# Performance work log

Hardware: AMD Instinct MI355X
Metric: run time of the kernel (lower is better)

The kernel has to match this reference:

```python
import jax, jax.numpy as jnp
import numpy as np

EMBED_DIM = 1024
NUM_HEADS = 16
HEAD_DIM = EMBED_DIM // NUM_HEADS


def setup_inputs() -> dict:
    key = jax.random.key(0)
    ks = jax.random.split(key, 5)
    s = 0.02
    return {
        "x": jax.random.normal(ks[0], (2, 2048, EMBED_DIM), dtype=jnp.float32),
        "w_qkv": jax.random.normal(ks[1], (EMBED_DIM, 3 * EMBED_DIM), dtype=jnp.float32) * s,
        "b_qkv": jnp.zeros((3 * EMBED_DIM,), dtype=jnp.float32),
        "w_out": jax.random.normal(ks[2], (EMBED_DIM, EMBED_DIM), dtype=jnp.float32) * s,
        "b_out": jnp.zeros((EMBED_DIM,), dtype=jnp.float32),
    }


def reference(x, w_qkv, b_qkv, w_out, b_out):
    B, T, C = x.shape
    qkv = x @ w_qkv + b_qkv                       # [B,T,3C]
    q, k, v = jnp.split(qkv, 3, axis=-1)
    # [B,T,C] -> [B,H,T,Dh]
    def heads(t):
        return t.reshape(B, T, NUM_HEADS, HEAD_DIM).transpose(0, 2, 1, 3)
    q, k, v = heads(q), heads(k), heads(v)
    scale = 1.0 / np.sqrt(HEAD_DIM).astype(np.float32)
    scores = jnp.einsum("bhqd,bhkd->bhqk", q, k) * scale  # [B,H,T,T]
    causal = jnp.tril(jnp.ones((T, T), dtype=bool))
    scores = jnp.where(causal[None, None], scores, -jnp.inf)
    attn = jax.nn.softmax(scores, axis=-1)
    out = jnp.einsum("bhqk,bhkd->bhqd", attn, v)  # [B,H,T,Dh]
    out = out.transpose(0, 2, 1, 3).reshape(B, T, C)
    return out @ w_out + b_out
```

## Files before the change

### kernel.cpp

```cpp
#include <hip/hip_runtime.h>

typedef unsigned short u16;
typedef unsigned int u32;
typedef __attribute__((ext_vector_type(8))) short bf16x8;
typedef __attribute__((ext_vector_type(4))) float f32x4;
typedef __attribute__((ext_vector_type(16))) float f32x16;

#define TOK   4096
#define EMB   1024
#define NQKV  3072
#define TSEQ  2048
#define NH    16

__device__ __forceinline__ u16 f2b(float f) {
  union { float f; unsigned u; } v; v.f = f;
  unsigned r = v.u + 0x7FFFu + ((v.u >> 16) & 1u);
  return (u16)(r >> 16);
}

__device__ __forceinline__ u32 pack_rn(float a, float b) {
  u32 ua = __float_as_uint(a) + 0x8000u;
  u32 ub = __float_as_uint(b) + 0x8000u;
  return __builtin_amdgcn_perm(ub, ua, 0x07060302u);
}

__device__ __forceinline__ f32x16 zero16() {
  f32x16 z;
#pragma unroll
  for (int i = 0; i < 16; i++) z[i] = 0.f;
  return z;
}


__global__ __launch_bounds__(256) void prep_kernel(const float* __restrict__ x,
                                                   u16* __restrict__ x_bf,
                                                   const float* __restrict__ w_qkv,
                                                   u16* __restrict__ wqkvT,
                                                   const float* __restrict__ w_out,
                                                   u16* __restrict__ woutT) {
  __shared__ u16 sm[64][65];
  int bid = blockIdx.x, tid = threadIdx.x;
  if (bid < 4096) {
    int i = bid * 256 + tid;
    float4 v = ((const float4*)x)[i];
    union { u16 us[4]; uint2 u2; } o;
    o.us[0] = f2b(v.x); o.us[1] = f2b(v.y); o.us[2] = f2b(v.z); o.us[3] = f2b(v.w);
    ((uint2*)x_bf)[i] = o.u2;
    return;
  }
  const float* src; u16* dst; int R, C, bx, by;
  if (bid < 4096 + 768) {
    int t = bid - 4096; bx = t % 48; by = t / 48;
    src = w_qkv; dst = wqkvT; R = EMB; C = NQKV;
  } else {
    int t = bid - 4096 - 768; bx = t & 15; by = t >> 4;
    src = w_out; dst = woutT; R = EMB; C = EMB;
  }
  int c0 = bx * 64, r0 = by * 64;
#pragma unroll
  for (int i = 0; i < 16; i++) {
    int idx = tid + i * 256;
    int r = idx >> 6, c = idx & 63;
    sm[r][c] = f2b(src[(size_t)(r0 + r) * C + c0 + c]);
  }
  __syncthreads();
#pragma unroll
  for (int i = 0; i < 16; i++) {
    int idx = tid + i * 256;
    int cc = idx >> 6, rr = idx & 63;
    dst[(size_t)(c0 + cc) * R + r0 + rr] = sm[rr][cc];
  }
}

__global__ __launch_bounds__(256) void transpose_v(const u16* __restrict__ V,
                                                   u16* __restrict__ Vt) {
  __shared__ u16 sm[64][72];
  int t0 = blockIdx.x * 64, bh = blockIdx.y;
  size_t base = (size_t)bh * TSEQ * 64;
  int tid = threadIdx.x;
  int r = tid >> 2, c = (tid & 3) * 16;
  *(bf16x8*)&sm[r][c]     = *(const bf16x8*)&V[base + (size_t)(t0 + r) * 64 + c];
  *(bf16x8*)&sm[r][c + 8] = *(const bf16x8*)&V[base + (size_t)(t0 + r) * 64 + c + 8];
  __syncthreads();
  int d = tid >> 2, tc = (tid & 3) * 16;
  union { u16 us[16]; uint4 v4[2]; } o;
#pragma unroll
  for (int i = 0; i < 16; i++) o.us[i] = sm[tc + i][d];
  *(uint4*)&Vt[base + (size_t)d * TSEQ + t0 + tc]     = o.v4[0];
  *(uint4*)&Vt[base + (size_t)d * TSEQ + t0 + tc + 8] = o.v4[1];
}


template <int MODE, int TM>
__global__ __launch_bounds__(256) void gemm_bt(const u16* __restrict__ A,
                                               const u16* __restrict__ Bt,
                                               const float* __restrict__ bias,
                                               u16* __restrict__ qb, u16* __restrict__ kb,
                                               u16* __restrict__ vb, float* __restrict__ outp,
                                               int K, int N) {
  constexpr int LDA = 68;
  constexpr int CT = (TM == 128) ? 4 : 2;
  constexpr int AC = TM / 32;
  __shared__ u16 As[TM][LDA];
  __shared__ u16 Bs[128][LDA];
  int tid = threadIdx.x;
  int m0 = blockIdx.y * TM, n0 = blockIdx.x * 128;
  int lane = tid & 63, wid = tid >> 6;
  int wm = (TM == 128) ? (wid >> 1) * 64 : 0;
  int wn = (TM == 128) ? (wid & 1) * 64 : wid * 32;
  int l15 = lane & 15, quad = lane >> 4;
  int lrow = lane >> 3, lcol = (lane & 7) * 8;

  f32x4 acc[4][CT];
#pragma unroll
  for (int i = 0; i < 4; i++)
#pragma unroll
    for (int j = 0; j < CT; j++) acc[i][j] = (f32x4){0.f, 0.f, 0.f, 0.f};

  bf16x8 ar[AC], br[4];
#pragma unroll
  for (int i = 0; i < AC; i++)
    ar[i] = *(const bf16x8*)&A[(size_t)(m0 + (wid * AC + i) * 8 + lrow) * K + lcol];
#pragma unroll
  for (int i = 0; i < 4; i++)
    br[i] = *(const bf16x8*)&Bt[(size_t)(n0 + (wid * 4 + i) * 8 + lrow) * K + lcol];

  for (int k0 = 0; k0 < K; k0 += 64) {
#pragma unroll
    for (int i = 0; i < AC; i++)
      *(bf16x8*)&As[(wid * AC + i) * 8 + lrow][lcol] = ar[i];
#pragma unroll
    for (int i = 0; i < 4; i++)
      *(bf16x8*)&Bs[(wid * 4 + i) * 8 + lrow][lcol] = br[i];
    __syncthreads();

    if (k0 + 64 < K) {
      int kn = k0 + 64;
#pragma unroll
      for (int i = 0; i < AC; i++)
        ar[i] = *(const bf16x8*)&A[(size_t)(m0 + (wid * AC + i) * 8 + lrow) * K + kn + lcol];
#pragma unroll
      for (int i = 0; i < 4; i++)
        br[i] = *(const bf16x8*)&Bt[(size_t)(n0 + (wid * 4 + i) * 8 + lrow) * K + kn + lcol];
    }

#pragma unroll
    for (int ks = 0; ks < 2; ks++) {
      bf16x8 af[4], bfr[CT];
#pragma unroll
      for (int rt = 0; rt < 4; rt++)
        af[rt] = *(const bf16x8*)&As[wm + rt * 16 + l15][ks * 32 + quad * 8];
#pragma unroll
      for (int ct = 0; ct < CT; ct++)
        bfr[ct] = *(const bf16x8*)&Bs[wn + ct * 16 + l15][ks * 32 + quad * 8];
#pragma unroll
      for (int rt = 0; rt < 4; rt++)
#pragma unroll
        for (int ct = 0; ct < CT; ct++)
          acc[rt][ct] = __builtin_amdgcn_mfma_f32_16x16x32_bf16(bfr[ct], af[rt], acc[rt][ct], 0, 0, 0);
    }
    __syncthreads();
  }

#pragma unroll
  for (int rt = 0; rt < 4; rt++) {
#pragma unroll
    for (int ct = 0; ct < CT; ct++) {
      int m = m0 + wm + rt * 16 + l15;
      int nb = n0 + wn + ct * 16 + quad * 4;
      float4 b4 = *(const float4*)&bias[nb];
      float v0 = acc[rt][ct][0] + b4.x, v1 = acc[rt][ct][1] + b4.y;
      float v2 = acc[rt][ct][2] + b4.z, v3 = acc[rt][ct][3] + b4.w;
      if (MODE == 0) {
        int sel = nb >> 10;
        int c = nb & 1023;
        int h = c >> 6, d0 = c & 63;
        int b = m >> 11, t = m & 2047;
        u16* dst = (sel == 0) ? qb : (sel == 1) ? kb : vb;
        union { u32 u[2]; uint2 u2; } o;
        o.u[0] = pack_rn(v0, v1);
        o.u[1] = pack_rn(v2, v3);
        *(uint2*)&dst[((((size_t)b * NH + h) * TSEQ + t) << 6) + d0] = o.u2;
      } else {
        float4 o = {v0, v1, v2, v3};
        *(float4*)&outp[(size_t)m * N + nb] = o;
      }
    }
  }
}


__global__ __launch_bounds__(128) void attn_kernel(const u16* __restrict__ Qb,
                                                   const u16* __restrict__ Kb,
                                                   const u16* __restrict__ Vtb,
                                                   u16* __restrict__ O) {
  __shared__ u16 Ks[64][68];
  __shared__ u16 Vt[64][68];
  __shared__ u16 Ps[2][32][36];

  const float SCL = 0.18033688f;
  const float MOFF = 16.0f;

  int id = blockIdx.x;
  int bh = (id >> 5) & 31;
  int q5 = id & 31;
  int qt = ((id >> 8) & 1) ? (31 - q5) : q5;

  int tid = threadIdx.x, lane = tid & 63, w = tid >> 6;
  int l31 = lane & 31, h = lane >> 5;
  const size_t hoff = (size_t)bh * TSEQ * 64;

  int qw = qt * 64 + w * 32;
  int qg = qw + l31;

  bf16x8 qf[4];
  {
    const u16* qp = Qb + hoff + (size_t)qg * 64 + h * 8;
#pragma unroll
    for (int s = 0; s < 4; s++) qf[s] = *(const bf16x8*)(qp + s * 16);
  }

  f32x16 acc[2];
  acc[0] = zero16(); acc[1] = zero16();
  float l_i = 0.f;

  int r = tid >> 1, cb = (tid & 1) * 32;
  bf16x8 kr[4], vr[4];
  {
    const u16* kg = Kb + hoff + (size_t)r * 64 + cb;
    const u16* vg = Vtb + hoff + (size_t)r * TSEQ + cb;
#pragma unroll
    for (int c = 0; c < 4; c++) {
      kr[c] = *(const bf16x8*)(kg + c * 8);
      vr[c] = *(const bf16x8*)(vg + c * 8);
    }
  }

  for (int kt = 0; kt <= qt; kt++) {
    __syncthreads();
#pragma unroll
    for (int c = 0; c < 4; c++) {
      *(bf16x8*)&Ks[r][cb + c * 8] = kr[c];
      *(bf16x8*)&Vt[r][cb + c * 8] = vr[c];
    }
    __syncthreads();
    if (kt < qt) {
      const u16* kg = Kb + hoff + (size_t)((kt + 1) * 64 + r) * 64 + cb;
      const u16* vg = Vtb + hoff + (size_t)r * TSEQ + (kt + 1) * 64 + cb;
#pragma unroll
      for (int c = 0; c < 4; c++) {
        kr[c] = *(const bf16x8*)(kg + c * 8);
        vr[c] = *(const bf16x8*)(vg + c * 8);
      }
    }

    int kb64 = kt * 64;
#pragma unroll
    for (int t = 0; t < 2; t++) {
      int kbt = kb64 + t * 32;
      if (kbt > qw + 31) continue;

      f32x16 sacc = zero16();
#pragma unroll
      for (int s = 0; s < 4; s++) {
        bf16x8 kf = *(const bf16x8*)&Ks[t * 32 + l31][s * 16 + h * 8];
        sacc = __builtin_amdgcn_mfma_f32_32x32x16_bf16(kf, qf[s], sacc, 0, 0, 0);
      }

      if (kbt + 31 > qw) {
#pragma unroll
        for (int rr = 0; rr < 16; rr++) {
          int key = kbt + (rr & 3) + 8 * (rr >> 2) + 4 * h;
          if (key > qg) sacc[rr] = -1e30f;
        }
      }

#pragma unroll
      for (int rr = 0; rr < 16; rr++) {
        float p = exp2f(__builtin_fmaf(sacc[rr], SCL, -MOFF));
        sacc[rr] = p;
        l_i += p;
      }

#pragma unroll
      for (int G = 0; G < 4; G++) {
        union { u32 u[2]; uint2 u2; } o;
        o.u[0] = pack_rn(sacc[4 * G + 0], sacc[4 * G + 1]);
        o.u[1] = pack_rn(sacc[4 * G + 2], sacc[4 * G + 3]);
        *(uint2*)&Ps[w][l31][G * 8 + 4 * h] = o.u2;
      }

#pragma unroll
      for (int s2 = 0; s2 < 2; s2++) {
        union { bf16x8 v; uint2 d[2]; } pu;
        pu.d[0] = *(const uint2*)&Ps[w][l31][s2 * 16 + h * 8];
        pu.d[1] = *(const uint2*)&Ps[w][l31][s2 * 16 + h * 8 + 4];
#pragma unroll
        for (int dt = 0; dt < 2; dt++) {
          bf16x8 vf = *(const bf16x8*)&Vt[dt * 32 + l31][t * 32 + s2 * 16 + h * 8];
          acc[dt] = __builtin_amdgcn_mfma_f32_32x32x16_bf16(vf, pu.v, acc[dt], 0, 0, 0);
        }
      }
    }
  }

  l_i += __shfl_xor(l_i, 32);
  float inv = 1.0f / l_i;

  int b = bh >> 4, head = bh & 15;
  size_t rowbase = ((size_t)b * TSEQ + qg) * 1024 + head * 64;
#pragma unroll
  for (int dt = 0; dt < 2; dt++)
#pragma unroll
    for (int G = 0; G < 4; G++) {
      union { u32 u[2]; uint2 u2; } o;
      o.u[0] = pack_rn(acc[dt][4 * G + 0] * inv, acc[dt][4 * G + 1] * inv);
      o.u[1] = pack_rn(acc[dt][4 * G + 2] * inv, acc[dt][4 * G + 3] * inv);
      *(uint2*)&O[rowbase + dt * 32 + G * 8 + 4 * h] = o.u2;
    }
}


extern "C" void kernel_launch(void* const* d_in, const int* in_sizes, int n_in,
                              void* d_out, int out_size, void* d_ws, size_t ws_size,
                              hipStream_t stream) {
  (void)in_sizes; (void)n_in; (void)out_size; (void)ws_size;
  const float* x     = (const float*)d_in[0];
  const float* w_qkv = (const float*)d_in[1];
  const float* b_qkv = (const float*)d_in[2];
  const float* w_out = (const float*)d_in[3];
  const float* b_out = (const float*)d_in[4];
  float* out = (float*)d_out;

  char* p = (char*)d_ws;
  u16* x_bf  = (u16*)p; p += (size_t)TOK * EMB * 2;
  u16* wqkvT = (u16*)p; p += (size_t)NQKV * EMB * 2;
  u16* woutT = (u16*)p; p += (size_t)EMB * EMB * 2;
  u16* Qb    = (u16*)p; p += (size_t)32 * TSEQ * 64 * 2;
  u16* Kb    = (u16*)p; p += (size_t)32 * TSEQ * 64 * 2;
  u16* Vraw  = (u16*)p; p += (size_t)32 * TSEQ * 64 * 2;
  u16* attn_o = (u16*)p;
  u16* Vtb   = x_bf;

  prep_kernel<<<dim3(4096 + 768 + 256), 256, 0, stream>>>(x, x_bf, w_qkv, wqkvT, w_out, woutT);
  gemm_bt<0, 128><<<dim3(NQKV / 128, TOK / 128), 256, 0, stream>>>(x_bf, wqkvT, b_qkv,
                                                                   Qb, Kb, Vraw, nullptr, EMB, NQKV);
  transpose_v<<<dim3(TSEQ / 64, 32), 256, 0, stream>>>(Vraw, Vtb);
  attn_kernel<<<dim3(1024), 128, 0, stream>>>(Qb, Kb, Vtb, attn_o);
  gemm_bt<1, 64><<<dim3(EMB / 128, TOK / 64), 256, 0, stream>>>(attn_o, woutT, b_out,
                                                                nullptr, nullptr, nullptr, out, EMB, EMB);
}
```

Measured before the change: 211.9 us.

## Split key tiles across four waves per attention block and reduce partials

The attention block grows from 2 to 4 waves. Each query half now has two waves, each taking one 32-key half of every 64-key tile, and their partial outputs and row sums are combined through shared memory at the end. The P matrix is rearranged into MFMA operand layout with cross-half lane shuffles instead of a round trip through shared memory. This aims for more parallelism and latency hiding per block, at the cost of a final shared-memory reduction, extra LDS and more waves sharing each tile.

```diff
diff --git a/kernel.cpp b/kernel.cpp
--- a/kernel.cpp
+++ b/kernel.cpp
@@ -190,13 +190,14 @@
 }
 
 
-__global__ __launch_bounds__(128) void attn_kernel(const u16* __restrict__ Qb,
-                                                   const u16* __restrict__ Kb,
-                                                   const u16* __restrict__ Vtb,
-                                                   u16* __restrict__ O) {
+__global__ __launch_bounds__(256, 4) void attn_kernel(const u16* __restrict__ Qb,
+                                                      const u16* __restrict__ Kb,
+                                                      const u16* __restrict__ Vtb,
+                                                      u16* __restrict__ O) {
   __shared__ u16 Ks[64][68];
   __shared__ u16 Vt[64][68];
-  __shared__ u16 Ps[2][32][36];
+  __shared__ float Cmb[2][16][64][2];
+  __shared__ float Lmb[2][32];
 
   const float SCL = 0.18033688f;
   const float MOFF = 16.0f;
@@ -207,10 +208,11 @@
   int qt = ((id >> 8) & 1) ? (31 - q5) : q5;
 
   int tid = threadIdx.x, lane = tid & 63, w = tid >> 6;
+  int sub = w & 1, par = w >> 1;
   int l31 = lane & 31, h = lane >> 5;
   const size_t hoff = (size_t)bh * TSEQ * 64;
 
-  int qw = qt * 64 + w * 32;
+  int qw = qt * 64 + sub * 32;
   int qg = qw + l31;
 
   bf16x8 qf[4];
@@ -224,46 +226,35 @@
   acc[0] = zero16(); acc[1] = zero16();
   float l_i = 0.f;
 
-  int r = tid >> 1, cb = (tid & 1) * 32;
-  bf16x8 kr[4], vr[4];
+  int r = tid >> 2, cb = (tid & 3) * 16;
+  bf16x8 kr0, kr1, vr0, vr1;
   {
     const u16* kg = Kb + hoff + (size_t)r * 64 + cb;
     const u16* vg = Vtb + hoff + (size_t)r * TSEQ + cb;
-#pragma unroll
-    for (int c = 0; c < 4; c++) {
-      kr[c] = *(const bf16x8*)(kg + c * 8);
-      vr[c] = *(const bf16x8*)(vg + c * 8);
-    }
+    kr0 = *(const bf16x8*)kg;       kr1 = *(const bf16x8*)(kg + 8);
+    vr0 = *(const bf16x8*)vg;       vr1 = *(const bf16x8*)(vg + 8);
   }
 
   for (int kt = 0; kt <= qt; kt++) {
     __syncthreads();
-#pragma unroll
-    for (int c = 0; c < 4; c++) {
-      *(bf16x8*)&Ks[r][cb + c * 8] = kr[c];
-      *(bf16x8*)&Vt[r][cb + c * 8] = vr[c];
-    }
+    *(bf16x8*)&Ks[r][cb]     = kr0;
+    *(bf16x8*)&Ks[r][cb + 8] = kr1;
+    *(bf16x8*)&Vt[r][cb]     = vr0;
+    *(bf16x8*)&Vt[r][cb + 8] = vr1;
     __syncthreads();
     if (kt < qt) {
       const u16* kg = Kb + hoff + (size_t)((kt + 1) * 64 + r) * 64 + cb;
       const u16* vg = Vtb + hoff + (size_t)r * TSEQ + (kt + 1) * 64 + cb;
-#pragma unroll
-      for (int c = 0; c < 4; c++) {
-        kr[c] = *(const bf16x8*)(kg + c * 8);
-        vr[c] = *(const bf16x8*)(vg + c * 8);
-      }
-    }
-
-    int kb64 = kt * 64;
-#pragma unroll
-    for (int t = 0; t < 2; t++) {
-      int kbt = kb64 + t * 32;
-      if (kbt > qw + 31) continue;
-
+      kr0 = *(const bf16x8*)kg;     kr1 = *(const bf16x8*)(kg + 8);
+      vr0 = *(const bf16x8*)vg;     vr1 = *(const bf16x8*)(vg + 8);
+    }
+
+    int kbt = kt * 64 + par * 32;
+    if (kbt <= qw + 31) {
       f32x16 sacc = zero16();
 #pragma unroll
       for (int s = 0; s < 4; s++) {
-        bf16x8 kf = *(const bf16x8*)&Ks[t * 32 + l31][s * 16 + h * 8];
+        bf16x8 kf = *(const bf16x8*)&Ks[par * 32 + l31][s * 16 + h * 8];
         sacc = __builtin_amdgcn_mfma_f32_32x32x16_bf16(kf, qf[s], sacc, 0, 0, 0);
       }
 
@@ -283,41 +274,65 @@
       }
 
 #pragma unroll
+      for (int s2 = 0; s2 < 2; s2++) {
+        u32 u0 = pack_rn(sacc[8 * s2 + 0], sacc[8 * s2 + 1]);
+        u32 u1 = pack_rn(sacc[8 * s2 + 2], sacc[8 * s2 + 3]);
+        u32 u2 = pack_rn(sacc[8 * s2 + 4], sacc[8 * s2 + 5]);
+        u32 u3 = pack_rn(sacc[8 * s2 + 6], sacc[8 * s2 + 7]);
+        u32 s0 = h ? u0 : u2, s1 = h ? u1 : u3;
+        u32 t0 = (u32)__shfl_xor((int)s0, 32);
+        u32 t1 = (u32)__shfl_xor((int)s1, 32);
+        union { u32 d[4]; bf16x8 v; } pf;
+        pf.d[0] = h ? t0 : u0;
+        pf.d[1] = h ? t1 : u1;
+        pf.d[2] = h ? u2 : t0;
+        pf.d[3] = h ? u3 : t1;
+#pragma unroll
+        for (int dt = 0; dt < 2; dt++) {
+          bf16x8 vf = *(const bf16x8*)&Vt[dt * 32 + l31][par * 32 + s2 * 16 + h * 8];
+          acc[dt] = __builtin_amdgcn_mfma_f32_32x32x16_bf16(vf, pf.v, acc[dt], 0, 0, 0);
+        }
+      }
+    }
+  }
+
+  l_i += __shfl_xor(l_i, 32);
+
+  __syncthreads();
+  if (par == 1) {
+#pragma unroll
+    for (int dt = 0; dt < 2; dt++)
+#pragma unroll
+      for (int pr = 0; pr < 8; pr++) {
+        Cmb[sub][dt * 8 + pr][lane][0] = acc[dt][2 * pr];
+        Cmb[sub][dt * 8 + pr][lane][1] = acc[dt][2 * pr + 1];
+      }
+    if (h == 0) Lmb[sub][l31] = l_i;
+  }
+  __syncthreads();
+  if (par == 0) {
+#pragma unroll
+    for (int dt = 0; dt < 2; dt++)
+#pragma unroll
+      for (int pr = 0; pr < 8; pr++) {
+        acc[dt][2 * pr]     += Cmb[sub][dt * 8 + pr][lane][0];
+        acc[dt][2 * pr + 1] += Cmb[sub][dt * 8 + pr][lane][1];
+      }
+    float lt = l_i + Lmb[sub][l31];
+    float inv = 1.0f / lt;
+
+    int b = bh >> 4, head = bh & 15;
+    size_t rowbase = ((size_t)b * TSEQ + qg) * 1024 + head * 64;
+#pragma unroll
+    for (int dt = 0; dt < 2; dt++)
+#pragma unroll
       for (int G = 0; G < 4; G++) {
         union { u32 u[2]; uint2 u2; } o;
-        o.u[0] = pack_rn(sacc[4 * G + 0], sacc[4 * G + 1]);
-        o.u[1] = pack_rn(sacc[4 * G + 2], sacc[4 * G + 3]);
-        *(uint2*)&Ps[w][l31][G * 8 + 4 * h] = o.u2;
-      }
-
-#pragma unroll
-      for (int s2 = 0; s2 < 2; s2++) {
-        union { bf16x8 v; uint2 d[2]; } pu;
-        pu.d[0] = *(const uint2*)&Ps[w][l31][s2 * 16 + h * 8];
-        pu.d[1] = *(const uint2*)&Ps[w][l31][s2 * 16 + h * 8 + 4];
-#pragma unroll
-        for (int dt = 0; dt < 2; dt++) {
-          bf16x8 vf = *(const bf16x8*)&Vt[dt * 32 + l31][t * 32 + s2 * 16 + h * 8];
-          acc[dt] = __builtin_amdgcn_mfma_f32_32x32x16_bf16(vf, pu.v, acc[dt], 0, 0, 0);
-        }
-      }
-    }
-  }
-
-  l_i += __shfl_xor(l_i, 32);
-  float inv = 1.0f / l_i;
-
-  int b = bh >> 4, head = bh & 15;
-  size_t rowbase = ((size_t)b * TSEQ + qg) * 1024 + head * 64;
-#pragma unroll
-  for (int dt = 0; dt < 2; dt++)
-#pragma unroll
-    for (int G = 0; G < 4; G++) {
-      union { u32 u[2]; uint2 u2; } o;
-      o.u[0] = pack_rn(acc[dt][4 * G + 0] * inv, acc[dt][4 * G + 1] * inv);
-      o.u[1] = pack_rn(acc[dt][4 * G + 2] * inv, acc[dt][4 * G + 3] * inv);
-      *(uint2*)&O[rowbase + dt * 32 + G * 8 + 4 * h] = o.u2;
-    }
+        o.u[0] = pack_rn(acc[dt][4 * G + 0] * inv, acc[dt][4 * G + 1] * inv);
+        o.u[1] = pack_rn(acc[dt][4 * G + 2] * inv, acc[dt][4 * G + 3] * inv);
+        *(uint2*)&O[rowbase + dt * 32 + G * 8 + 4 * h] = o.u2;
+      }
+  }
 }
 
 
@@ -346,7 +361,7 @@
   gemm_bt<0, 128><<<dim3(NQKV / 128, TOK / 128), 256, 0, stream>>>(x_bf, wqkvT, b_qkv,
                                                                    Qb, Kb, Vraw, nullptr, EMB, NQKV);
   transpose_v<<<dim3(TSEQ / 64, 32), 256, 0, stream>>>(Vraw, Vtb);
-  attn_kernel<<<dim3(1024), 128, 0, stream>>>(Qb, Kb, Vtb, attn_o);
+  attn_kernel<<<dim3(1024), 256, 0, stream>>>(Qb, Kb, Vtb, attn_o);
   gemm_bt<1, 64><<<dim3(EMB / 128, TOK / 64), 256, 0, stream>>>(attn_o, woutT, b_out,
                                                                 nullptr, nullptr, nullptr, out, EMB, EMB);
 }
```

Measured after the change: 186.5 us. -12.0%, faster.
